# Optimization experiments

Hardware: AMD Instinct MI355X
Metric: run time of the kernel (lower is better)

Reference implementation:

```python
import jax, jax.numpy as jnp
import numpy as np

WINDOW_SIZE = 11
SIGMA = 1.5
C_IN = 3

def _gaussian_window():
    coords = jnp.arange(WINDOW_SIZE, dtype=jnp.float32) - WINDOW_SIZE // 2
    g = jnp.exp(-(coords ** 2) / (2.0 * SIGMA ** 2))
    g = g / g.sum()
    win = g[:, None] * g[None, :]                       # [11, 11]
    return jnp.broadcast_to(win[None, None], (C_IN, 1, WINDOW_SIZE, WINDOW_SIZE))

def _depthwise_conv(x, w):
    pad = WINDOW_SIZE // 2
    return jax.lax.conv_general_dilated(
        x, w,
        window_strides=(1, 1),
        padding=[(pad, pad), (pad, pad)],
        dimension_numbers=('NCHW', 'OIHW', 'NCHW'),
        feature_group_count=C_IN)

def setup_inputs() -> dict:
    key = jax.random.key(0)
    k1, k2 = jax.random.split(key)
    clean = jax.random.uniform(k1, (32, 3, 512, 512), dtype=jnp.float32)
    adversarial = jax.random.uniform(k2, (32, 3, 512, 512), dtype=jnp.float32)
    return {"clean": clean, "adversarial": adversarial}

def reference(clean, adversarial):
    C1 = 0.01 ** 2
    C2 = 0.03 ** 2
    w = _gaussian_window()
    mu1 = _depthwise_conv(clean, w)
    mu2 = _depthwise_conv(adversarial, w)
    mu1_sq = mu1 ** 2
    mu2_sq = mu2 ** 2
    mu12 = mu1 * mu2
    sigma1_sq = _depthwise_conv(clean ** 2, w) - mu1_sq
    sigma2_sq = _depthwise_conv(adversarial ** 2, w) - mu2_sq
    sigma12 = _depthwise_conv(clean * adversarial, w) - mu12
    ssim_map = ((2.0 * mu12 + C1) * (2.0 * sigma12 + C2)) / (
        (mu1_sq + mu2_sq + C1) * (sigma1_sq + sigma2_sq + C2))
    return 1.0 - ssim_map.mean()
```

## Files before the change

### kernel.cpp

```cpp
#include <hip/hip_runtime.h>


typedef float v2f __attribute__((ext_vector_type(2)));
typedef float v4f __attribute__((ext_vector_type(4)));

#define IMG 512
#define TILE 64
#define HALO 5
#define LROWS 74
#define LCOLS 74
#define LSTRIDE 76
#define LSTRIDE4 38
#define RPT 4
#define NPIX 25165824.0

__device__ constexpr float WT[11] = {
    0.00102838f, 0.00759876f, 0.03600077f, 0.10936068f, 0.21300552f,
    0.26601173f,
    0.21300552f, 0.10936068f, 0.03600077f, 0.00759876f, 0.00102838f};

__global__ __launch_bounds__(512)
__attribute__((amdgpu_waves_per_eu(6, 6)))
void ssim_main(const float* __restrict__ clean,
               const float* __restrict__ adv,
               double* __restrict__ accum)
{
    __shared__ __align__(16) v2f tile[LROWS * LSTRIDE];
    __shared__ float wpart[8];

    const int tid = threadIdx.x;
    const int b = blockIdx.x;
    const int plane = b >> 6;
    const int t6 = b & 63;
    const int tile_x = (t6 & 7) * TILE;
    const int tile_y = (t6 >> 3) * TILE;

    const float* __restrict__ cp = clean + (size_t)plane * (IMG * IMG);
    const float* __restrict__ ap = adv   + (size_t)plane * (IMG * IMG);

    for (int idx = tid; idx < LROWS * LCOLS; idx += 512) {
        int r = idx / LCOLS;
        int c = idx - r * LCOLS;
        int gr = tile_y + r - HALO;
        int gc = tile_x + c - HALO;
        v2f v = {0.f, 0.f};
        if (gr >= 0 && gr < IMG && gc >= 0 && gc < IMG) {
            int gi = gr * IMG + gc;
            float x = cp[gi];
            float y = ap[gi];
            v.x = x + y;
            v.y = x - y;
        }
        tile[r * LSTRIDE + c] = v;
    }
    __syncthreads();

    const int cpair = tid & 31;
    const int strip = tid >> 5;
    const int r0 = strip * RPT;
    const v4f* __restrict__ tile4 = (const v4f*)tile;

    v2f aA0[RPT], aA1[RPT], aB0[RPT], aB1[RPT];
    #pragma unroll
    for (int o = 0; o < RPT; ++o) {
        aA0[o] = (v2f){0.f, 0.f}; aA1[o] = (v2f){0.f, 0.f};
        aB0[o] = (v2f){0.f, 0.f}; aB1[o] = (v2f){0.f, 0.f};
    }

    #pragma unroll
    for (int j = 0; j < RPT + 10; ++j) {
        const v4f* bp = tile4 + (r0 + j) * LSTRIDE4 + cpair;
        v4f q0 = bp[0], q1 = bp[1], q2 = bp[2], q3 = bp[3], q4 = bp[4], q5 = bp[5];
        v2f t[12];
        t[0]  = (v2f){q0.x, q0.y}; t[1]  = (v2f){q0.z, q0.w};
        t[2]  = (v2f){q1.x, q1.y}; t[3]  = (v2f){q1.z, q1.w};
        t[4]  = (v2f){q2.x, q2.y}; t[5]  = (v2f){q2.z, q2.w};
        t[6]  = (v2f){q3.x, q3.y}; t[7]  = (v2f){q3.z, q3.w};
        t[8]  = (v2f){q4.x, q4.y}; t[9]  = (v2f){q4.z, q4.w};
        t[10] = (v2f){q5.x, q5.y}; t[11] = (v2f){q5.z, q5.w};

        v2f hA0 = {0.f, 0.f}, hA1 = {0.f, 0.f};
        v2f hB0 = {0.f, 0.f}, hB1 = {0.f, 0.f};
        #pragma unroll
        for (int k = 0; k < 12; ++k) {
            v2f tv = t[k];
            v2f pp = tv * tv;
            if (k < 11) {
                const float w = WT[k];
                hA0 += w * tv; hB0 += w * pp;
            }
            if (k > 0) {
                const float w = WT[k - 1];
                hA1 += w * tv; hB1 += w * pp;
            }
        }

        #pragma unroll
        for (int o = 0; o < RPT; ++o) {
            const int kv = j - o;
            if (kv >= 0 && kv < 11) {
                const float w = WT[kv];
                aA0[o] += w * hA0; aA1[o] += w * hA1;
                aB0[o] += w * hB0; aB1[o] += w * hB1;
            }
        }
    }

    const float C1 = 1e-4f;
    const float C2 = 9e-4f;
    float lsum = 0.f;
    #pragma unroll
    for (int o = 0; o < RPT; ++o) {
        #pragma unroll
        for (int s = 0; s < 2; ++s) {
            v2f a  = s ? aA1[o] : aA0[o];
            v2f bb = s ? aB1[o] : aB0[o];
            float U = a.x * a.x;
            float V = a.y * a.y;
            float halfUmV = 0.5f * (U - V);
            float halfUpV = 0.5f * (U + V);
            float num1 = halfUmV + C1;
            float num2 = 0.5f * (bb.x - bb.y) - halfUmV + C2;
            float den1 = halfUpV + C1;
            float den2 = 0.5f * (bb.x + bb.y) - halfUpV + C2;
            lsum += (num1 * num2) * __builtin_amdgcn_rcpf(den1 * den2);
        }
    }

    #pragma unroll
    for (int off = 32; off > 0; off >>= 1)
        lsum += __shfl_down(lsum, off);
    const int lane = tid & 63;
    const int wave = tid >> 6;
    if (lane == 0) wpart[wave] = lsum;
    __syncthreads();
    if (tid == 0) {
        float bs = 0.f;
        #pragma unroll
        for (int w = 0; w < 8; ++w) bs += wpart[w];
        atomicAdd(accum, (double)bs);
    }
}

__global__ void ssim_finalize(const double* __restrict__ accum,
                              float* __restrict__ out)
{
    if (threadIdx.x == 0) {
        out[0] = 1.f - (float)(accum[0] / NPIX);
    }
}

extern "C" void kernel_launch(void* const* d_in, const int* in_sizes, int n_in,
                              void* d_out, int out_size, void* d_ws, size_t ws_size,
                              hipStream_t stream)
{
    const float* clean = (const float*)d_in[0];
    const float* adv   = (const float*)d_in[1];
    float* out = (float*)d_out;
    double* accum = (double*)d_ws;

    hipMemsetAsync(accum, 0, sizeof(double), stream);

    const int nblocks = 96 * 64;
    ssim_main<<<nblocks, 512, 0, stream>>>(clean, adv, accum);
    ssim_finalize<<<1, 64, 0, stream>>>(accum, out);
}
```

Measured before the change: 311.6 us.

## Stream full-width row strips with a rolling register window for the vertical pass

```diff
diff --git a/kernel.cpp b/kernel.cpp
--- a/kernel.cpp
+++ b/kernel.cpp
@@ -2,139 +2,133 @@
 
 
 typedef float v2f __attribute__((ext_vector_type(2)));
-typedef float v4f __attribute__((ext_vector_type(4)));
 
 #define IMG 512
-#define TILE 64
-#define HALO 5
-#define LROWS 74
-#define LCOLS 74
-#define LSTRIDE 76
-#define LSTRIDE4 38
-#define RPT 4
+#define BH 32
+#define BUFW 522
 #define NPIX 25165824.0
+#define C1f 1e-4f
+#define C2f 9e-4f
 
-__device__ constexpr float WT[11] = {
-    0.00102838f, 0.00759876f, 0.03600077f, 0.10936068f, 0.21300552f,
-    0.26601173f,
-    0.21300552f, 0.10936068f, 0.03600077f, 0.00759876f, 0.00102838f};
+#define W0  0.00102838f
+#define W1  0.00759876f
+#define W2  0.03600077f
+#define W3  0.10936068f
+#define W4  0.21300552f
+#define W5  0.26601173f
+#define W6  0.21300552f
+#define W7  0.10936068f
+#define W8  0.03600077f
+#define W9  0.00759876f
+#define W10 0.00102838f
+
+#define STEP(S, a0,a1,a2,a3,a4,a5,a6,a7,a8,a9,a10) { \
+    const int j = jj * 11 + (S); \
+    float px = 0.f, py = 0.f; \
+    { const int gr = by + j - 4;              \
+      if ((unsigned)gr < (unsigned)IMG) { \
+          const int gi = (gr << 9) + c; px = cp[gi]; py = ap[gi]; } } \
+    __syncthreads(); \
+    (((S) & 1) ? q0 : q1)[c + 5] = (v2f){px + py, px - py}; \
+    { const v2f* rb = ((S) & 1) ? q1 : q0; \
+      v2f t, hA, hB; \
+      t = rb[c+0];  hA  = W0*t;  hB  = W0*(t*t); \
+      t = rb[c+1];  hA += W1*t;  hB += W1*(t*t); \
+      t = rb[c+2];  hA += W2*t;  hB += W2*(t*t); \
+      t = rb[c+3];  hA += W3*t;  hB += W3*(t*t); \
+      t = rb[c+4];  hA += W4*t;  hB += W4*(t*t); \
+      t = rb[c+5];  hA += W5*t;  hB += W5*(t*t); \
+      t = rb[c+6];  hA += W6*t;  hB += W6*(t*t); \
+      t = rb[c+7];  hA += W7*t;  hB += W7*(t*t); \
+      t = rb[c+8];  hA += W8*t;  hB += W8*(t*t); \
+      t = rb[c+9];  hA += W9*t;  hB += W9*(t*t); \
+      t = rb[c+10]; hA += W10*t; hB += W10*(t*t); \
+      wA##S = hA; wB##S = hB; } \
+    if (j >= 10 && j < 10 + BH) { \
+      v2f vA = W0*wA##a0 + W1*wA##a1 + W2*wA##a2 + W3*wA##a3 + W4*wA##a4 \
+             + W5*wA##a5 + W6*wA##a6 + W7*wA##a7 + W8*wA##a8 + W9*wA##a9 \
+             + W10*wA##a10; \
+      v2f vB = W0*wB##a0 + W1*wB##a1 + W2*wB##a2 + W3*wB##a3 + W4*wB##a4 \
+             + W5*wB##a5 + W6*wB##a6 + W7*wB##a7 + W8*wB##a8 + W9*wB##a9 \
+             + W10*wB##a10; \
+      const float U = vA.x * vA.x, V = vA.y * vA.y; \
+      const float hUmV = 0.5f * (U - V); \
+      const float hUpV = 0.5f * (U + V); \
+      const float n1 = hUmV + C1f; \
+      const float n2 = 0.5f * (vB.x - vB.y) - hUmV + C2f; \
+      const float d1 = hUpV + C1f; \
+      const float d2 = 0.5f * (vB.x + vB.y) - hUpV + C2f; \
+      lsum += (n1 * n2) * __builtin_amdgcn_rcpf(d1 * d2); } }
 
 __global__ __launch_bounds__(512)
-__attribute__((amdgpu_waves_per_eu(6, 6)))
+__attribute__((amdgpu_waves_per_eu(4, 4)))
 void ssim_main(const float* __restrict__ clean,
                const float* __restrict__ adv,
                double* __restrict__ accum)
 {
-    __shared__ __align__(16) v2f tile[LROWS * LSTRIDE];
+    __shared__ __align__(16) v2f buf0[BUFW];
+    __shared__ __align__(16) v2f buf1[BUFW];
     __shared__ float wpart[8];
 
-    const int tid = threadIdx.x;
+    const int c = threadIdx.x;
     const int b = blockIdx.x;
-    const int plane = b >> 6;
-    const int t6 = b & 63;
-    const int tile_x = (t6 & 7) * TILE;
-    const int tile_y = (t6 >> 3) * TILE;
+    const int plane = b >> 4;
+    const int by = (b & 15) * BH;
 
     const float* __restrict__ cp = clean + (size_t)plane * (IMG * IMG);
     const float* __restrict__ ap = adv   + (size_t)plane * (IMG * IMG);
 
-    for (int idx = tid; idx < LROWS * LCOLS; idx += 512) {
-        int r = idx / LCOLS;
-        int c = idx - r * LCOLS;
-        int gr = tile_y + r - HALO;
-        int gc = tile_x + c - HALO;
-        v2f v = {0.f, 0.f};
-        if (gr >= 0 && gr < IMG && gc >= 0 && gc < IMG) {
-            int gi = gr * IMG + gc;
-            float x = cp[gi];
-            float y = ap[gi];
-            v.x = x + y;
-            v.y = x - y;
-        }
-        tile[r * LSTRIDE + c] = v;
-    }
-    __syncthreads();
-
-    const int cpair = tid & 31;
-    const int strip = tid >> 5;
-    const int r0 = strip * RPT;
-    const v4f* __restrict__ tile4 = (const v4f*)tile;
-
-    v2f aA0[RPT], aA1[RPT], aB0[RPT], aB1[RPT];
-    #pragma unroll
-    for (int o = 0; o < RPT; ++o) {
-        aA0[o] = (v2f){0.f, 0.f}; aA1[o] = (v2f){0.f, 0.f};
-        aB0[o] = (v2f){0.f, 0.f}; aB1[o] = (v2f){0.f, 0.f};
+    if (c < 10) {
+        const int hi = (c < 5) ? c : (512 + c);
+        buf0[hi] = (v2f){0.f, 0.f};
+        buf1[hi] = (v2f){0.f, 0.f};
     }
 
-    #pragma unroll
-    for (int j = 0; j < RPT + 10; ++j) {
-        const v4f* bp = tile4 + (r0 + j) * LSTRIDE4 + cpair;
-        v4f q0 = bp[0], q1 = bp[1], q2 = bp[2], q3 = bp[3], q4 = bp[4], q5 = bp[5];
-        v2f t[12];
-        t[0]  = (v2f){q0.x, q0.y}; t[1]  = (v2f){q0.z, q0.w};
-        t[2]  = (v2f){q1.x, q1.y}; t[3]  = (v2f){q1.z, q1.w};
-        t[4]  = (v2f){q2.x, q2.y}; t[5]  = (v2f){q2.z, q2.w};
-        t[6]  = (v2f){q3.x, q3.y}; t[7]  = (v2f){q3.z, q3.w};
-        t[8]  = (v2f){q4.x, q4.y}; t[9]  = (v2f){q4.z, q4.w};
-        t[10] = (v2f){q5.x, q5.y}; t[11] = (v2f){q5.z, q5.w};
+    v2f* q0 = buf0;
+    v2f* q1 = buf1;
 
-        v2f hA0 = {0.f, 0.f}, hA1 = {0.f, 0.f};
-        v2f hB0 = {0.f, 0.f}, hB1 = {0.f, 0.f};
-        #pragma unroll
-        for (int k = 0; k < 12; ++k) {
-            v2f tv = t[k];
-            v2f pp = tv * tv;
-            if (k < 11) {
-                const float w = WT[k];
-                hA0 += w * tv; hB0 += w * pp;
-            }
-            if (k > 0) {
-                const float w = WT[k - 1];
-                hA1 += w * tv; hB1 += w * pp;
-            }
+    {
+        const int gr = by - 5;
+        float x = 0.f, y = 0.f;
+        if ((unsigned)gr < (unsigned)IMG) {
+            const int gi = (gr << 9) + c;
+            x = cp[gi]; y = ap[gi];
         }
-
-        #pragma unroll
-        for (int o = 0; o < RPT; ++o) {
-            const int kv = j - o;
-            if (kv >= 0 && kv < 11) {
-                const float w = WT[kv];
-                aA0[o] += w * hA0; aA1[o] += w * hA1;
-                aB0[o] += w * hB0; aB1[o] += w * hB1;
-            }
-        }
+        q0[c + 5] = (v2f){x + y, x - y};
     }
 
-    const float C1 = 1e-4f;
-    const float C2 = 9e-4f;
+    v2f wA0={0.f,0.f}, wA1={0.f,0.f}, wA2={0.f,0.f}, wA3={0.f,0.f};
+    v2f wA4={0.f,0.f}, wA5={0.f,0.f}, wA6={0.f,0.f}, wA7={0.f,0.f};
+    v2f wA8={0.f,0.f}, wA9={0.f,0.f}, wA10={0.f,0.f};
+    v2f wB0={0.f,0.f}, wB1={0.f,0.f}, wB2={0.f,0.f}, wB3={0.f,0.f};
+    v2f wB4={0.f,0.f}, wB5={0.f,0.f}, wB6={0.f,0.f}, wB7={0.f,0.f};
+    v2f wB8={0.f,0.f}, wB9={0.f,0.f}, wB10={0.f,0.f};
+
     float lsum = 0.f;
-    #pragma unroll
-    for (int o = 0; o < RPT; ++o) {
-        #pragma unroll
-        for (int s = 0; s < 2; ++s) {
-            v2f a  = s ? aA1[o] : aA0[o];
-            v2f bb = s ? aB1[o] : aB0[o];
-            float U = a.x * a.x;
-            float V = a.y * a.y;
-            float halfUmV = 0.5f * (U - V);
-            float halfUpV = 0.5f * (U + V);
-            float num1 = halfUmV + C1;
-            float num2 = 0.5f * (bb.x - bb.y) - halfUmV + C2;
-            float den1 = halfUpV + C1;
-            float den2 = 0.5f * (bb.x + bb.y) - halfUpV + C2;
-            lsum += (num1 * num2) * __builtin_amdgcn_rcpf(den1 * den2);
-        }
+
+    for (int jj = 0; jj < 4; ++jj) {
+        STEP(0,  1,2,3,4,5,6,7,8,9,10,0)
+        STEP(1,  2,3,4,5,6,7,8,9,10,0,1)
+        STEP(2,  3,4,5,6,7,8,9,10,0,1,2)
+        STEP(3,  4,5,6,7,8,9,10,0,1,2,3)
+        STEP(4,  5,6,7,8,9,10,0,1,2,3,4)
+        STEP(5,  6,7,8,9,10,0,1,2,3,4,5)
+        STEP(6,  7,8,9,10,0,1,2,3,4,5,6)
+        STEP(7,  8,9,10,0,1,2,3,4,5,6,7)
+        STEP(8,  9,10,0,1,2,3,4,5,6,7,8)
+        STEP(9,  10,0,1,2,3,4,5,6,7,8,9)
+        STEP(10, 0,1,2,3,4,5,6,7,8,9,10)
+        v2f* tq = q0; q0 = q1; q1 = tq;
     }
 
     #pragma unroll
     for (int off = 32; off > 0; off >>= 1)
         lsum += __shfl_down(lsum, off);
-    const int lane = tid & 63;
-    const int wave = tid >> 6;
+    const int lane = c & 63;
+    const int wave = c >> 6;
     if (lane == 0) wpart[wave] = lsum;
     __syncthreads();
-    if (tid == 0) {
+    if (c == 0) {
         float bs = 0.f;
         #pragma unroll
         for (int w = 0; w < 8; ++w) bs += wpart[w];
@@ -161,7 +155,7 @@
 
     hipMemsetAsync(accum, 0, sizeof(double), stream);
 
-    const int nblocks = 96 * 64;
+    const int nblocks = 96 * 16;
     ssim_main<<<nblocks, 512, 0, stream>>>(clean, adv, accum);
     ssim_finalize<<<1, 64, 0, stream>>>(accum, out);
 }
```

After: 752.8 us. 142% more time.
